# Kernel optimization log

Measured on AMD Instinct MI355X. Metric: run time of the kernel, lower is better.

Reference implementation:

```python
import jax, jax.numpy as jnp
import numpy as np
import math

B, H, S, D = 2, 16, 2048, 64

def setup_inputs() -> dict:
    key = jax.random.key(0)
    kq, kk, kv = jax.random.split(key, 3)
    Q = jax.random.normal(kq, (B, H, S, D), dtype=jnp.float32)
    K = jax.random.normal(kk, (B, H, S, D), dtype=jnp.float32)
    V = jax.random.normal(kv, (B, H, S, D), dtype=jnp.float32)
    causal_mask = jnp.tril(jnp.ones((S, S), dtype=bool))
    return {"Q": Q, "K": K, "V": V, "causal_mask": causal_mask}

def reference(Q, K, V, causal_mask):
    d_k = K.shape[-1]
    scores = jnp.einsum('bhqd,bhkd->bhqk', Q, K) / math.sqrt(d_k)
    scores = jnp.where(causal_mask, scores, -jnp.inf)
    probs = jax.nn.softmax(scores, axis=-1)
    return jnp.einsum('bhqk,bhkd->bhqd', probs, V)
```

## Files before the change

kernel.cpp:

```cpp
#include <hip/hip_runtime.h>
#include <math.h>


constexpr int kS  = 2048;
constexpr int kD  = 64;
constexpr int kBH = 32;
constexpr int kPad = 72;

typedef __attribute__((ext_vector_type(8))) short short8;
typedef __attribute__((ext_vector_type(4))) float float4v;

static __device__ inline unsigned short f2bf(float f) {
  union { float f; unsigned u; } v; v.f = f;
  unsigned r = v.u + 0x7FFF + ((v.u >> 16) & 1);
  return (unsigned short)(r >> 16);
}

static __device__ inline short8 pack8(float4v a, float4v b) {
  short8 r;
  r[0] = (short)f2bf(a[0]); r[1] = (short)f2bf(a[1]);
  r[2] = (short)f2bf(a[2]); r[3] = (short)f2bf(a[3]);
  r[4] = (short)f2bf(b[0]); r[5] = (short)f2bf(b[1]);
  r[6] = (short)f2bf(b[2]); r[7] = (short)f2bf(b[3]);
  return r;
}

__global__ __launch_bounds__(256)
void prep_kernel(const float* __restrict__ K, const float* __restrict__ V,
                 unsigned short* __restrict__ Kb, unsigned short* __restrict__ VT) {
  __shared__ unsigned short tile[64 * kPad];
  const int tid = threadIdx.x;
  const int bh = blockIdx.y, st = blockIdx.x;
  const size_t ibase = (size_t)bh * kS * kD + (size_t)st * 64 * kD;
  const int r  = tid >> 2;
  const int c0 = (tid & 3) * 16;

  {
    const float* kp = K + ibase + (size_t)r * kD + c0;
    float4v a = *(const float4v*)(kp);
    float4v b = *(const float4v*)(kp + 4);
    float4v c = *(const float4v*)(kp + 8);
    float4v d = *(const float4v*)(kp + 12);
    unsigned short* dst = Kb + ibase + (size_t)r * kD + c0;
    *(short8*)dst       = pack8(a, b);
    *(short8*)(dst + 8) = pack8(c, d);
  }
  {
    const float* vp = V + ibase + (size_t)r * kD + c0;
    float4v a = *(const float4v*)(vp);
    float4v b = *(const float4v*)(vp + 4);
    float4v c = *(const float4v*)(vp + 8);
    float4v d = *(const float4v*)(vp + 12);
    unsigned short* t = &tile[r * kPad + c0];
    *(short8*)t       = pack8(a, b);
    *(short8*)(t + 8) = pack8(c, d);
  }
  __syncthreads();
  {
    const int dd = tid >> 2;
    const int s0 = (tid & 3) * 16;
    short8 w0, w1;
    #pragma unroll
    for (int i = 0; i < 8; ++i) {
      w0[i] = (short)tile[(s0 + i) * kPad + dd];
      w1[i] = (short)tile[(s0 + 8 + i) * kPad + dd];
    }
    unsigned short* vdst = VT + (size_t)bh * kD * kS + (size_t)dd * kS + st * 64 + s0;
    *(short8*)vdst       = w0;
    *(short8*)(vdst + 8) = w1;
  }
}

__global__ __launch_bounds__(256)
void fattn_kernel(const float* __restrict__ Q, const unsigned short* __restrict__ Kb,
                  const unsigned short* __restrict__ VT, float* __restrict__ O) {
  __shared__ __align__(16) unsigned short ldsK[64 * kPad];
  __shared__ __align__(16) unsigned short ldsVT[64 * kPad];
  __shared__ __align__(16) unsigned short ldsP[4 * 16 * kPad];

  const int tid  = threadIdx.x;
  const int wave = tid >> 6;
  const int lane = tid & 63;
  const int ln   = lane & 15;
  const int quad = lane >> 4;

  const int bh = blockIdx.y;
  const int qi = gridDim.x - 1 - blockIdx.x;
  const int q0 = qi * 64;
  const int wq0 = q0 + wave * 16;

  const size_t base = (size_t)bh * kS * kD;

  short8 qf[2];
  {
    const float scl = 0.125f * 1.44269504089f;
    const float* qp = Q + base + (size_t)(wq0 + ln) * kD + quad * 8;
    #pragma unroll
    for (int h = 0; h < 2; ++h) {
      float4v a = *(const float4v*)(qp + h * 32);
      float4v b = *(const float4v*)(qp + h * 32 + 4);
      #pragma unroll
      for (int i = 0; i < 4; ++i) { a[i] *= scl; b[i] *= scl; }
      qf[h] = pack8(a, b);
    }
  }

  short8 ones;
  #pragma unroll
  for (int i = 0; i < 8; ++i) ones[i] = (short)0x3F80;

  float4v acc[4] = {{0,0,0,0},{0,0,0,0},{0,0,0,0},{0,0,0,0}};
  float4v lacc   = {0,0,0,0};

  const int srow = tid >> 2;
  const int sc0  = (tid & 3) * 16;
  const unsigned short* Kg = Kb + base + (size_t)srow * kD + sc0;
  const unsigned short* Vg = VT + (size_t)bh * kD * kS + (size_t)srow * kS + sc0;

  const int nkt = qi + 1;

  short8 pk0 = *(const short8*)(Kg);
  short8 pk1 = *(const short8*)(Kg + 8);
  short8 pv0 = *(const short8*)(Vg);
  short8 pv1 = *(const short8*)(Vg + 8);

  for (int kt = 0; kt < nkt; ++kt) {
    const int kb = kt * 64;
    __syncthreads();
    {
      unsigned short* kd = &ldsK[srow * kPad + sc0];
      *(short8*)kd       = pk0;
      *(short8*)(kd + 8) = pk1;
      unsigned short* vd = &ldsVT[srow * kPad + sc0];
      *(short8*)vd       = pv0;
      *(short8*)(vd + 8) = pv1;
    }
    __syncthreads();
    if (kt + 1 < nkt) {
      Kg += 64 * kD;
      Vg += 64;
      pk0 = *(const short8*)(Kg);
      pk1 = *(const short8*)(Kg + 8);
      pv0 = *(const short8*)(Vg);
      pv1 = *(const short8*)(Vg + 8);
    }

    float4v s4[4];
    #pragma unroll
    for (int ct = 0; ct < 4; ++ct) {
      const unsigned short* kro = &ldsK[(ct * 16 + ln) * kPad + quad * 8];
      short8 k0 = *(const short8*)(kro);
      short8 k1 = *(const short8*)(kro + 32);
      float4v z = {0.f, 0.f, 0.f, 0.f};
      z = __builtin_amdgcn_mfma_f32_16x16x32_bf16(qf[0], k0, z, 0, 0, 0);
      z = __builtin_amdgcn_mfma_f32_16x16x32_bf16(qf[1], k1, z, 0, 0, 0);
      s4[ct] = z;
    }

    if (kb + 63 > wq0) {
      #pragma unroll
      for (int ct = 0; ct < 4; ++ct) {
        const int kg = kb + ct * 16 + ln;
        #pragma unroll
        for (int r = 0; r < 4; ++r) {
          if (kg > wq0 + quad * 4 + r) s4[ct][r] = -1e30f;
        }
      }
    }

    unsigned short* pw = &ldsP[wave * 16 * kPad];
    #pragma unroll
    for (int ct = 0; ct < 4; ++ct) {
      #pragma unroll
      for (int r = 0; r < 4; ++r) {
        float p = __builtin_amdgcn_exp2f(s4[ct][r]);
        pw[(quad * 4 + r) * kPad + ct * 16 + ln] =
            (unsigned short)(__float_as_uint(p) >> 16);
      }
    }
    const unsigned short* prd = pw + ln * kPad + quad * 8;
    short8 pf0 = *(const short8*)(prd);
    short8 pf1 = *(const short8*)(prd + 32);

    #pragma unroll
    for (int dt = 0; dt < 4; ++dt) {
      const unsigned short* vr = &ldsVT[(dt * 16 + ln) * kPad + quad * 8];
      short8 v0 = *(const short8*)(vr);
      short8 v1 = *(const short8*)(vr + 32);
      acc[dt] = __builtin_amdgcn_mfma_f32_16x16x32_bf16(pf0, v0, acc[dt], 0, 0, 0);
      acc[dt] = __builtin_amdgcn_mfma_f32_16x16x32_bf16(pf1, v1, acc[dt], 0, 0, 0);
    }
    lacc = __builtin_amdgcn_mfma_f32_16x16x32_bf16(pf0, ones, lacc, 0, 0, 0);
    lacc = __builtin_amdgcn_mfma_f32_16x16x32_bf16(pf1, ones, lacc, 0, 0, 0);
  }

  #pragma unroll
  for (int r = 0; r < 4; ++r) {
    const float inv = 1.f / lacc[r];
    const int qg = wq0 + quad * 4 + r;
    float* op = O + base + (size_t)qg * kD + ln;
    #pragma unroll
    for (int dt = 0; dt < 4; ++dt) op[dt * 16] = acc[dt][r] * inv;
  }
}

extern "C" void kernel_launch(void* const* d_in, const int* in_sizes, int n_in,
                              void* d_out, int out_size, void* d_ws, size_t ws_size,
                              hipStream_t stream) {
  const float* Q = (const float*)d_in[0];
  const float* K = (const float*)d_in[1];
  const float* V = (const float*)d_in[2];
  float* O = (float*)d_out;

  unsigned short* Kb = (unsigned short*)d_ws;
  unsigned short* VT = Kb + (size_t)kBH * kS * kD;

  dim3 grid(kS / 64, kBH);
  prep_kernel<<<grid, 256, 0, stream>>>(K, V, Kb, VT);
  fattn_kernel<<<grid, 256, 0, stream>>>(Q, Kb, VT, O);
}
```

Measured before the change: 163.4 us.

## Switch attention to 32x32 MFMA with 128-row query tiles per block

Each block now covers 128 query rows, 32 per wave, instead of 64, and uses 32x32x16 bf16 MFMA for both QK^T and PV in place of 16x16x32. The row-sum is accumulated in registers from the exp values rather than through extra MFMAs against a ones vector, then combined across half-waves with a shuffle and through LDS. Each K/V tile loaded into LDS is reused by twice as many query rows, and fully masked 32-column subtiles are skipped per wave. The cost is half as many blocks, which makes the causal workload imbalance coarser, plus more registers per wave.

```diff
diff --git a/kernel.cpp b/kernel.cpp
--- a/kernel.cpp
+++ b/kernel.cpp
@@ -6,9 +6,12 @@
 constexpr int kD  = 64;
 constexpr int kBH = 32;
 constexpr int kPad = 72;
-
-typedef __attribute__((ext_vector_type(8))) short short8;
-typedef __attribute__((ext_vector_type(4))) float float4v;
+constexpr int kBQ  = 128;
+
+typedef short short8 __attribute__((ext_vector_type(8)));
+typedef float float4v __attribute__((ext_vector_type(4)));
+typedef float float16v __attribute__((ext_vector_type(16)));
+typedef unsigned short ushort4v __attribute__((ext_vector_type(4)));
 
 static __device__ inline unsigned short f2bf(float f) {
   union { float f; unsigned u; } v; v.f = f;
@@ -34,7 +37,6 @@
   const size_t ibase = (size_t)bh * kS * kD + (size_t)st * 64 * kD;
   const int r  = tid >> 2;
   const int c0 = (tid & 3) * 16;
-
   {
     const float* kp = K + ibase + (size_t)r * kD + c0;
     float4v a = *(const float4v*)(kp);
@@ -76,53 +78,54 @@
                   const unsigned short* __restrict__ VT, float* __restrict__ O) {
   __shared__ __align__(16) unsigned short ldsK[64 * kPad];
   __shared__ __align__(16) unsigned short ldsVT[64 * kPad];
-  __shared__ __align__(16) unsigned short ldsP[4 * 16 * kPad];
+  __shared__ __align__(16) unsigned short ldsP[4 * 32 * kPad];
+  __shared__ float ldsL[4 * 32];
 
   const int tid  = threadIdx.x;
   const int wave = tid >> 6;
   const int lane = tid & 63;
-  const int ln   = lane & 15;
-  const int quad = lane >> 4;
+  const int l31  = lane & 31;
+  const int h    = lane >> 5;
 
   const int bh = blockIdx.y;
   const int qi = gridDim.x - 1 - blockIdx.x;
-  const int q0 = qi * 64;
-  const int wq0 = q0 + wave * 16;
+  const int q0 = qi * kBQ;
+  const int wq0 = q0 + wave * 32;
 
   const size_t base = (size_t)bh * kS * kD;
 
-  short8 qf[2];
+  short8 qf[4];
   {
     const float scl = 0.125f * 1.44269504089f;
-    const float* qp = Q + base + (size_t)(wq0 + ln) * kD + quad * 8;
+    const float* qp = Q + base + (size_t)(wq0 + l31) * kD + h * 8;
     #pragma unroll
-    for (int h = 0; h < 2; ++h) {
-      float4v a = *(const float4v*)(qp + h * 32);
-      float4v b = *(const float4v*)(qp + h * 32 + 4);
+    for (int dk = 0; dk < 4; ++dk) {
+      float4v a = *(const float4v*)(qp + dk * 16);
+      float4v b = *(const float4v*)(qp + dk * 16 + 4);
       #pragma unroll
       for (int i = 0; i < 4; ++i) { a[i] *= scl; b[i] *= scl; }
-      qf[h] = pack8(a, b);
-    }
-  }
-
-  short8 ones;
+      qf[dk] = pack8(a, b);
+    }
+  }
+
+  float16v acc0, acc1;
   #pragma unroll
-  for (int i = 0; i < 8; ++i) ones[i] = (short)0x3F80;
-
-  float4v acc[4] = {{0,0,0,0},{0,0,0,0},{0,0,0,0},{0,0,0,0}};
-  float4v lacc   = {0,0,0,0};
+  for (int i = 0; i < 16; ++i) { acc0[i] = 0.f; acc1[i] = 0.f; }
+  float lacc = 0.f;
 
   const int srow = tid >> 2;
   const int sc0  = (tid & 3) * 16;
   const unsigned short* Kg = Kb + base + (size_t)srow * kD + sc0;
   const unsigned short* Vg = VT + (size_t)bh * kD * kS + (size_t)srow * kS + sc0;
 
-  const int nkt = qi + 1;
+  const int nkt = 2 * qi + 2;
 
   short8 pk0 = *(const short8*)(Kg);
   short8 pk1 = *(const short8*)(Kg + 8);
   short8 pv0 = *(const short8*)(Vg);
   short8 pv1 = *(const short8*)(Vg + 8);
+
+  unsigned short* pw = &ldsP[wave * 32 * kPad + l31 * kPad];
 
   for (int kt = 0; kt < nkt; ++kt) {
     const int kb = kt * 64;
@@ -145,62 +148,65 @@
       pv1 = *(const short8*)(Vg + 8);
     }
 
-    float4v s4[4];
     #pragma unroll
-    for (int ct = 0; ct < 4; ++ct) {
-      const unsigned short* kro = &ldsK[(ct * 16 + ln) * kPad + quad * 8];
-      short8 k0 = *(const short8*)(kro);
-      short8 k1 = *(const short8*)(kro + 32);
-      float4v z = {0.f, 0.f, 0.f, 0.f};
-      z = __builtin_amdgcn_mfma_f32_16x16x32_bf16(qf[0], k0, z, 0, 0, 0);
-      z = __builtin_amdgcn_mfma_f32_16x16x32_bf16(qf[1], k1, z, 0, 0, 0);
-      s4[ct] = z;
-    }
-
-    if (kb + 63 > wq0) {
-      #pragma unroll
-      for (int ct = 0; ct < 4; ++ct) {
-        const int kg = kb + ct * 16 + ln;
+    for (int kt32 = 0; kt32 < 2; ++kt32) {
+      const int ktb = kb + kt32 * 32;
+      if (ktb > wq0 + 31) break;
+
+      float16v s;
+      #pragma unroll
+      for (int i = 0; i < 16; ++i) s[i] = 0.f;
+      const unsigned short* kro = &ldsK[(kt32 * 32 + l31) * kPad + h * 8];
+      #pragma unroll
+      for (int dk = 0; dk < 4; ++dk) {
+        short8 kf = *(const short8*)(kro + dk * 16);
+        s = __builtin_amdgcn_mfma_f32_32x32x16_bf16(kf, qf[dk], s, 0, 0, 0);
+      }
+
+      if (ktb + 31 > wq0) {
+        const int qg = wq0 + l31;
         #pragma unroll
-        for (int r = 0; r < 4; ++r) {
-          if (kg > wq0 + quad * 4 + r) s4[ct][r] = -1e30f;
+        for (int r = 0; r < 16; ++r) {
+          const int kg = ktb + (r & 3) + 8 * (r >> 2) + 4 * h;
+          if (kg > qg) s[r] = -1e30f;
         }
       }
-    }
-
-    unsigned short* pw = &ldsP[wave * 16 * kPad];
-    #pragma unroll
-    for (int ct = 0; ct < 4; ++ct) {
-      #pragma unroll
-      for (int r = 0; r < 4; ++r) {
-        float p = __builtin_amdgcn_exp2f(s4[ct][r]);
-        pw[(quad * 4 + r) * kPad + ct * 16 + ln] =
-            (unsigned short)(__float_as_uint(p) >> 16);
-      }
-    }
-    const unsigned short* prd = pw + ln * kPad + quad * 8;
-    short8 pf0 = *(const short8*)(prd);
-    short8 pf1 = *(const short8*)(prd + 32);
-
-    #pragma unroll
-    for (int dt = 0; dt < 4; ++dt) {
-      const unsigned short* vr = &ldsVT[(dt * 16 + ln) * kPad + quad * 8];
-      short8 v0 = *(const short8*)(vr);
-      short8 v1 = *(const short8*)(vr + 32);
-      acc[dt] = __builtin_amdgcn_mfma_f32_16x16x32_bf16(pf0, v0, acc[dt], 0, 0, 0);
-      acc[dt] = __builtin_amdgcn_mfma_f32_16x16x32_bf16(pf1, v1, acc[dt], 0, 0, 0);
-    }
-    lacc = __builtin_amdgcn_mfma_f32_16x16x32_bf16(pf0, ones, lacc, 0, 0, 0);
-    lacc = __builtin_amdgcn_mfma_f32_16x16x32_bf16(pf1, ones, lacc, 0, 0, 0);
-  }
-
+
+      #pragma unroll
+      for (int rb = 0; rb < 4; ++rb) {
+        ushort4v w;
+        #pragma unroll
+        for (int i = 0; i < 4; ++i) {
+          float p = __builtin_amdgcn_exp2f(s[rb * 4 + i]);
+          lacc += p;
+          w[i] = (unsigned short)(__float_as_uint(p) >> 16);
+        }
+        *(ushort4v*)(pw + kt32 * 32 + rb * 8 + 4 * h) = w;
+      }
+
+      #pragma unroll
+      for (int kc2 = 0; kc2 < 2; ++kc2) {
+        const int ko = kt32 * 32 + kc2 * 16;
+        short8 pf  = *(const short8*)(pw + ko + h * 8);
+        short8 vf0 = *(const short8*)(&ldsVT[l31 * kPad + ko + h * 8]);
+        short8 vf1 = *(const short8*)(&ldsVT[(32 + l31) * kPad + ko + h * 8]);
+        acc0 = __builtin_amdgcn_mfma_f32_32x32x16_bf16(pf, vf0, acc0, 0, 0, 0);
+        acc1 = __builtin_amdgcn_mfma_f32_32x32x16_bf16(pf, vf1, acc1, 0, 0, 0);
+      }
+    }
+  }
+
+  lacc += __shfl_xor(lacc, 32);
+  if (h == 0) ldsL[wave * 32 + l31] = lacc;
+  __syncthreads();
   #pragma unroll
-  for (int r = 0; r < 4; ++r) {
-    const float inv = 1.f / lacc[r];
-    const int qg = wq0 + quad * 4 + r;
-    float* op = O + base + (size_t)qg * kD + ln;
-    #pragma unroll
-    for (int dt = 0; dt < 4; ++dt) op[dt * 16] = acc[dt][r] * inv;
+  for (int r = 0; r < 16; ++r) {
+    const int row = (r & 3) + 8 * (r >> 2) + 4 * h;
+    const float inv = 1.f / ldsL[wave * 32 + row];
+    const int qg = wq0 + row;
+    float* op = O + base + (size_t)qg * kD + l31;
+    op[0]  = acc0[r] * inv;
+    op[32] = acc1[r] * inv;
   }
 }
 
@@ -215,7 +221,8 @@
   unsigned short* Kb = (unsigned short*)d_ws;
   unsigned short* VT = Kb + (size_t)kBH * kS * kD;
 
-  dim3 grid(kS / 64, kBH);
-  prep_kernel<<<grid, 256, 0, stream>>>(K, V, Kb, VT);
+  dim3 gprep(kS / 64, kBH);
+  prep_kernel<<<gprep, 256, 0, stream>>>(K, V, Kb, VT);
+  dim3 grid(kS / kBQ, kBH);
   fattn_kernel<<<grid, 256, 0, stream>>>(Q, Kb, VT, O);
 }
```

After: 150.1 us. 8.1% less time.
